# Kernel tuning notes

Measured on AMD Instinct MI355X. Metric: run time of the kernel, lower is better.

Reference implementation:

```python
import jax, jax.numpy as jnp
import numpy as np
import math

B, H, S, D = 2, 16, 2048, 72
D12 = D // 12  # freq dim per head per component
L_PREFIX, L_SEQ = 576, 512
THETA_T = 100.0


def _make_freqs():
    n = H * D12
    log_min, log_max = math.log(math.pi), math.log(10.0 * math.pi)
    f = jnp.exp(jnp.linspace(log_min, log_max, n + 1)[:-1])  # (H*D12,)
    freqs = jnp.stack([f, f]).reshape(2, D12, H)
    freqs = jnp.swapaxes(freqs, -1, -2)  # (2, H, D12)
    t = THETA_T ** (-jnp.arange(n, dtype=jnp.float32) / n)
    t_freqs = t.reshape(D12, H).T  # (H, D12)
    return freqs.astype(jnp.float32), t_freqs.astype(jnp.float32)


def setup_inputs() -> dict:
    key = jax.random.key(0)
    ks = jax.random.split(key, 8)
    freqs, t_freqs = _make_freqs()
    return {
        "q": jax.random.normal(ks[0], (B, H, S, D), dtype=jnp.float32),
        "k": jax.random.normal(ks[1], (B, H, S, D), dtype=jnp.float32),
        "v": jax.random.normal(ks[2], (B, H, S, D), dtype=jnp.float32),
        "pos": jax.random.uniform(ks[3], (B, S, 2), dtype=jnp.float32),
        "pos_orig": jax.random.uniform(ks[4], (B, S, 2), dtype=jnp.float32),
        "time": jax.random.uniform(ks[5], (B, S), dtype=jnp.float32),
        "freqs": freqs,
        "t_freqs": t_freqs,
        "scale": jax.random.uniform(ks[6], (H, 1, 1), dtype=jnpp_f32()) if False else jax.random.uniform(ks[6], (H, 1, 1), dtype=jnp.float32) + 0.5,
        "l_prefix": L_PREFIX,
        "l_seq": L_SEQ,
    }


def jnp_f32():
    return jnp.float32


def _fp_rope_theta(pos, pos_orig, time, freqs, t_freqs):
    # FPRoPE.forward: theta per token, per head. (B,S,H,5*D12)
    p = jnp.stack([pos_orig, pos], axis=2) * 2.0 - 1.0  # (B,S,2,2)
    th_w = p[..., 0][:, :, :, None, None] * freqs[0]  # (B,S,2,H,D12)
    th_h = p[..., 1][:, :, :, None, None] * freqs[1]  # (B,S,2,H,D12)
    th_t = time[:, :, None, None, None] * t_freqs      # (B,S,1,H,D12)
    theta = jnp.concatenate([th_h, th_w, th_t], axis=2)  # (B,S,5,H,D12)
    theta = jnp.transpose(theta, (0, 3, 1, 2, 4)).reshape(B, H, S, 5 * D12)
    return theta


def _apply_rotary(x, theta):
    d = theta.shape[-1]
    x1, x2, x3 = x[..., :d], x[..., d:2 * d], x[..., 2 * d:]
    c, s = jnp.cos(theta), jnp.sin(theta)
    return jnp.concatenate([x1 * c - x2 * s, x2 * c + x1 * s, x3], axis=-1)


def _block_mask(l_prefix, l_seq):
    # inference_query_causal_mask_mod: prefix attends to nothing; pokes causal;
    # queries attend to prefix+pokes (and self via qn==kn).
    idx = jnp.arange(S)
    qn = (idx - l_prefix)[:, None]
    kn = (idx - l_prefix)[None, :]
    return (qn >= 0) & ((qn == kn) | ((qn >= kn) & (qn < l_seq)) | ((kn < l_seq) & (qn >= l_seq)))


def reference(q, k, v, pos, pos_orig, time, freqs, t_freqs, scale, l_prefix, l_seq):
    theta = _fp_rope_theta(pos, pos_orig, time, freqs, t_freqs)
    q = _apply_rotary(q, theta)
    k = _apply_rotary(k, theta)
    # cosine-similarity QK rescaling (scale_for_cosine_sim)
    eps = 1e-6
    ss = jnp.sqrt(scale)  # (H,1,1) broadcasts over (B,H,S,1)
    q = q * (ss * jax.lax.rsqrt(jnp.sum(q * q, axis=-1, keepdims=True) + eps))
    k = k * (ss * jax.lax.rsqrt(jnp.sum(k * k, axis=-1, keepdims=True) + eps))
    mask = _block_mask(l_prefix, l_seq)  # (S,S)
    scores = jnp.einsum('bhqd,bhkd->bhqk', q, k)
    scores = jnp.where(mask, scores, jnp.float32(-1e30))
    probs = jax.nn.softmax(scores, axis=-1)
    # fully-masked rows (prefix queries) output zeros, matching flex_attention
    row_valid = jnp.any(mask, axis=-1)  # (S,)
    probs = jnp.where(row_valid[None, None, :, None], probs, 0.0)
    return jnp.einsum('bhqk,bhkd->bhqd', probs, v)
```

## Files before the change

kernel.cpp:

```cpp
#include <hip/hip_runtime.h>
#include <math.h>

#define B_ 2
#define H_ 16
#define S_ 2048
#define D_ 72
#define LP 576
#define WEND 1088
#define DP 96
#define DV 80
#define NQ (S_ - LP)

#define CBW 5376
#define LDSW (CBW + 256 + 64)

#define NPREP2 (B_ * H_ * S_ / 8)
#define NVT    (32 * B_ * H_)

typedef __bf16 bf16x8 __attribute__((ext_vector_type(8)));
typedef float f32x4 __attribute__((ext_vector_type(4)));

static __device__ __forceinline__ unsigned pack2bf(float a, float b) {
    __bf16 x = (__bf16)a, y = (__bf16)b;
    unsigned short ux = __builtin_bit_cast(unsigned short, x);
    unsigned short uy = __builtin_bit_cast(unsigned short, y);
    return (unsigned)ux | ((unsigned)uy << 16);
}

static __device__ __forceinline__ f32x4 mfma16(bf16x8 a, bf16x8 b, f32x4 c) {
    return __builtin_amdgcn_mfma_f32_16x16x32_bf16(a, b, c, 0, 0, 0);
}

__global__ __launch_bounds__(256) void pre_kernel(
    const float* __restrict__ q, const float* __restrict__ k,
    const float* __restrict__ v,
    const float* __restrict__ pos, const float* __restrict__ pos_orig,
    const float* __restrict__ time_, const float* __restrict__ freqs,
    const float* __restrict__ t_freqs, const float* __restrict__ scale,
    unsigned* __restrict__ qn, unsigned* __restrict__ kn,
    unsigned short* __restrict__ vt, float* __restrict__ out)
{
    __shared__ __align__(16) float tile[64 * 77];
    if (blockIdx.x < NPREP2) {
        unsigned short* shp = (unsigned short*)tile;
        const int wave = threadIdx.x >> 6;
        const int lane = threadIdx.x & 63;
        const int j = lane & 31;
        const int rw = wave * 2 + (lane >> 5);
        const int row = blockIdx.x * 8 + rw;
        const int s = row & (S_ - 1);
        const int h = (row >> 11) & (H_ - 1);
        const int b = row >> 15;
        const long base = (long)row * D_;
        const int p2 = (b * S_ + s) * 2;

        float oq1 = 0.f, oq2 = 0.f, ok1 = 0.f, ok2 = 0.f;
        float pq[6], pk[6];
        float ssq = 0.f, ssk = 0.f;
        if (j < 30) {
            const float x1q = q[base + j], x2q = q[base + j + 30];
            const float x1k = k[base + j], x2k = k[base + j + 30];
            const int g = j / 6, i = j - 6 * g;
            const float fh = freqs[96 + h * 6 + i];
            const float fw = freqs[h * 6 + i];
            const float ft = t_freqs[h * 6 + i];
            const float f  = (g < 2) ? fh : ((g < 4) ? fw : ft);
            const float by_o = pos_orig[p2 + 1] * 2.f - 1.f;
            const float by_p = pos[p2 + 1]      * 2.f - 1.f;
            const float bx_o = pos_orig[p2 + 0] * 2.f - 1.f;
            const float bx_p = pos[p2 + 0]      * 2.f - 1.f;
            const float bt   = time_[b * S_ + s];
            const float bv = (g == 0) ? by_o : (g == 1) ? by_p :
                             (g == 2) ? bx_o : (g == 3) ? bx_p : bt;
            float sn, cs;
            __sincosf(bv * f, &sn, &cs);
            oq1 = x1q * cs - x2q * sn;  oq2 = x2q * cs + x1q * sn;
            ok1 = x1k * cs - x2k * sn;  ok2 = x2k * cs + x1k * sn;
            ssq = oq1 * oq1 + oq2 * oq2;
            ssk = ok1 * ok1 + ok2 * ok2;
        } else {
            const int e0 = 60 + 6 * (j - 30);
            #pragma unroll
            for (int m = 0; m < 3; ++m) {
                const float2 a = *(const float2*)(q + base + e0 + 2 * m);
                const float2 c = *(const float2*)(k + base + e0 + 2 * m);
                pq[2 * m] = a.x; pq[2 * m + 1] = a.y;
                pk[2 * m] = c.x; pk[2 * m + 1] = c.y;
                ssq += a.x * a.x + a.y * a.y;
                ssk += c.x * c.x + c.y * c.y;
            }
        }
        #pragma unroll
        for (int m = 1; m < 32; m <<= 1) { ssq += __shfl_xor(ssq, m); ssk += __shfl_xor(ssk, m); }
        const float ss = sqrtf(scale[h]);
        const float fq = ss * rsqrtf(ssq + 1e-6f);
        const float fk = ss * rsqrtf(ssk + 1e-6f);

        unsigned short* sq_ = shp + rw * 96;
        unsigned short* sk_ = shp + 768 + rw * 96;
        if (j < 30) {
            sq_[j]      = __builtin_bit_cast(unsigned short, (__bf16)(oq1 * fq));
            sq_[j + 30] = __builtin_bit_cast(unsigned short, (__bf16)(oq2 * fq));
            sk_[j]      = __builtin_bit_cast(unsigned short, (__bf16)(ok1 * fk));
            sk_[j + 30] = __builtin_bit_cast(unsigned short, (__bf16)(ok2 * fk));
        } else {
            const int e0 = 60 + 6 * (j - 30);
            #pragma unroll
            for (int m = 0; m < 6; ++m) {
                sq_[e0 + m] = __builtin_bit_cast(unsigned short, (__bf16)(pq[m] * fq));
                sk_[e0 + m] = __builtin_bit_cast(unsigned short, (__bf16)(pk[m] * fk));
            }
        }
        __syncthreads();
        const int t = threadIdx.x;
        if (t < 192) {
            const int arr = t / 96, rem = t - arr * 96;
            const int rr = rem / 12, seg = rem - rr * 12;
            uint4 val = make_uint4(0u, 0u, 0u, 0u);
            if (seg < 9) val = ((const uint4*)(shp + arr * 768 + rr * 96))[seg];
            unsigned* dst = (arr ? kn : qn) + ((long)(blockIdx.x * 8 + rr)) * 48;
            ((uint4*)dst)[seg] = val;
        }
    } else {
        const int bx2 = blockIdx.x - NPREP2;
        const int st = bx2 & 31, bh = bx2 >> 5;
        const int s0 = st * 64;
        const int t = threadIdx.x;
        if (st < 9) {
            float4* o4 = (float4*)(out + (long)(bh * S_ + s0) * D_);
            for (int i = t; i < 1152; i += 256) o4[i] = make_float4(0.f, 0.f, 0.f, 0.f);
        }
        for (int i = t; i < 1152; i += 256) {
            const int r = i / 18, c = i - r * 18;
            const float4 g = ((const float4*)v)[((long)(bh * S_ + s0 + r) * 18) + c];
            float* d = &tile[r * 77 + c * 4];
            d[0] = g.x; d[1] = g.y; d[2] = g.z; d[3] = g.w;
        }
        __syncthreads();
        for (int i = t; i < 1280; i += 256) {
            const int dd = i >> 4, s4 = i & 15;
            float f0 = 0.f, f1 = 0.f, f2 = 0.f, f3 = 0.f;
            if (dd < D_) {
                f0 = tile[(s4 * 4 + 0) * 77 + dd];
                f1 = tile[(s4 * 4 + 1) * 77 + dd];
                f2 = tile[(s4 * 4 + 2) * 77 + dd];
                f3 = tile[(s4 * 4 + 3) * 77 + dd];
            }
            uint2 o; o.x = pack2bf(f0, f1); o.y = pack2bf(f2, f3);
            ((uint2*)vt)[((((long)bh * DV + dd) << 11) + s0 + s4 * 4) >> 2] = o;
        }
    }
}

__global__ __launch_bounds__(256) void attn_kernel(
    const unsigned short* __restrict__ qn, const unsigned short* __restrict__ kn,
    const unsigned short* __restrict__ vt, float* __restrict__ out)
{
    __shared__ __align__(16) unsigned lds[LDSW];
    const int bh = blockIdx.y;
    const int q0 = LP + blockIdx.x * 64;
    const int tid = threadIdx.x;
    const int w = tid >> 6, lane = tid & 63;
    const int quad = lane >> 4, l16 = lane & 15;
    const bool causal = (q0 < WEND);
    const int ntiles = causal ? ((q0 + 191) >> 7) : 9;

    const unsigned short* qn_b = qn + (((long)bh) << 11) * DP;
    const unsigned short* kn_b = kn + (((long)bh) << 11) * DP;
    const unsigned short* vt_b = vt + (long)bh * DV * S_;

    bf16x8 qf[4][3];
    #pragma unroll
    for (int m = 0; m < 4; ++m)
        #pragma unroll
        for (int c = 0; c < 3; ++c)
            qf[m][c] = *(const bf16x8*)(qn_b + (long)(q0 + 16 * m + l16) * DP + c * 32 + quad * 8);

    f32x4 o[4][5];
    float den[4][4];
    #pragma unroll
    for (int m = 0; m < 4; ++m) {
        #pragma unroll
        for (int dt = 0; dt < 5; ++dt) { o[m][dt][0]=0.f; o[m][dt][1]=0.f; o[m][dt][2]=0.f; o[m][dt][3]=0.f; }
        #pragma unroll
        for (int r = 0; r < 4; ++r) den[m][r] = 0.f;
    }

    unsigned short* Pw = (unsigned short*)lds + w * 640;

    for (int kt = 0; kt < ntiles; ++kt) {
        const int kb = kt * 128 + 32 * w;
        bf16x8 kf[2][3], vf[5];
        #pragma unroll
        for (int g = 0; g < 2; ++g)
            #pragma unroll
            for (int c = 0; c < 3; ++c)
                kf[g][c] = *(const bf16x8*)(kn_b + (long)(kb + 16 * g + l16) * DP + c * 32 + quad * 8);
        #pragma unroll
        for (int dt = 0; dt < 5; ++dt)
            vf[dt] = *(const bf16x8*)(vt_b + (((long)(dt * 16 + l16)) << 11) + kb + quad * 8);

        #pragma unroll
        for (int m = 0; m < 4; ++m) {
            f32x4 acc0, acc1;
            acc0[0]=0.f; acc0[1]=0.f; acc0[2]=0.f; acc0[3]=0.f;
            acc1[0]=0.f; acc1[1]=0.f; acc1[2]=0.f; acc1[3]=0.f;
            #pragma unroll
            for (int c = 0; c < 3; ++c) {
                acc0 = mfma16(qf[m][c], kf[0][c], acc0);
                acc1 = mfma16(qf[m][c], kf[1][c], acc1);
            }
            #pragma unroll
            for (int g = 0; g < 2; ++g) {
                const int ka = kb + 16 * g + l16;
                #pragma unroll
                for (int r = 0; r < 4; ++r) {
                    const int qa = q0 + 16 * m + quad * 4 + r;
                    float p = g ? acc1[r] : acc0[r];
                    const bool valid = causal ? (ka <= qa) : (ka < WEND);
                    p = valid ? __expf(p) : 0.f;
                    const __bf16 pb = (__bf16)p;
                    den[m][r] += (float)pb;
                    Pw[(quad * 4 + r) * 40 + 16 * g + l16] = __builtin_bit_cast(unsigned short, pb);
                }
            }
            const bf16x8 pa = *(const bf16x8*)(Pw + l16 * 40 + quad * 8);
            #pragma unroll
            for (int dt = 0; dt < 5; ++dt)
                o[m][dt] = mfma16(pa, vf[dt], o[m][dt]);
        }
    }

    #pragma unroll
    for (int m = 0; m < 4; ++m)
        #pragma unroll
        for (int r = 0; r < 4; ++r)
            #pragma unroll
            for (int x = 1; x < 16; x <<= 1) den[m][r] += __shfl_xor(den[m][r], x);

    __syncthreads();
    float* cb  = (float*)lds;
    float* db  = (float*)lds + CBW;
    float* PsD = (float*)lds + CBW + 256;
    if (l16 == 0)
        #pragma unroll
        for (int m = 0; m < 4; ++m)
            #pragma unroll
            for (int r = 0; r < 4; ++r)
                db[w * 64 + 16 * m + quad * 4 + r] = den[m][r];

    float ofin[5][4];
    #pragma unroll
    for (int dt = 0; dt < 5; ++dt) {
        __syncthreads();
        #pragma unroll
        for (int m = 0; m < 4; ++m)
            #pragma unroll
            for (int r = 0; r < 4; ++r)
                cb[w * 1344 + (16 * m + quad * 4 + r) * 21 + l16] = o[m][dt][r];
        __syncthreads();
        #pragma unroll
        for (int r = 0; r < 4; ++r) {
            const int row = 16 * w + quad * 4 + r;
            ofin[dt][r] = cb[row * 21 + l16] + cb[1344 + row * 21 + l16]
                        + cb[2688 + row * 21 + l16] + cb[4032 + row * 21 + l16];
        }
    }
    float dfin[4];
    #pragma unroll
    for (int r = 0; r < 4; ++r) {
        const int row = 16 * w + quad * 4 + r;
        dfin[r] = db[row] + db[64 + row] + db[128 + row] + db[192 + row];
    }

    if (!causal) {
        bf16x8 qw[3];
        #pragma unroll
        for (int m = 0; m < 4; ++m)
            if (w == m) { qw[0] = qf[m][0]; qw[1] = qf[m][1]; qw[2] = qf[m][2]; }
        float sp = 0.f;
        #pragma unroll
        for (int c = 0; c < 3; ++c) {
            const bf16x8 kd = *(const bf16x8*)(kn_b + (long)(q0 + 16 * w + l16) * DP + c * 32 + quad * 8);
            #pragma unroll
            for (int j = 0; j < 8; ++j) sp += (float)qw[c][j] * (float)kd[j];
        }
        sp += __shfl_xor(sp, 16);
        sp += __shfl_xor(sp, 32);
        if (quad == 0) PsD[w * 16 + l16] = __expf(sp);
        #pragma unroll
        for (int r = 0; r < 4; ++r) {
            const float pd = PsD[w * 16 + quad * 4 + r];
            dfin[r] += pd;
            const int qa = q0 + 16 * w + quad * 4 + r;
            #pragma unroll
            for (int dt = 0; dt < 5; ++dt) {
                const unsigned short uv = vt_b[(((long)(dt * 16 + l16)) << 11) + qa];
                ofin[dt][r] += pd * (float)__builtin_bit_cast(__bf16, uv);
            }
        }
    }

    #pragma unroll
    for (int r = 0; r < 4; ++r) {
        const float inv = 1.f / dfin[r];
        const int qa = q0 + 16 * w + quad * 4 + r;
        float* orow = out + ((long)(bh * S_ + qa)) * D_;
        #pragma unroll
        for (int dt = 0; dt < 5; ++dt) {
            const int dim = dt * 16 + l16;
            if (dim < D_) orow[dim] = ofin[dt][r] * inv;
        }
    }
}

extern "C" void kernel_launch(void* const* d_in, const int* in_sizes, int n_in,
                              void* d_out, int out_size, void* d_ws, size_t ws_size,
                              hipStream_t stream) {
    const float* q        = (const float*)d_in[0];
    const float* k        = (const float*)d_in[1];
    const float* v        = (const float*)d_in[2];
    const float* pos      = (const float*)d_in[3];
    const float* pos_orig = (const float*)d_in[4];
    const float* time_    = (const float*)d_in[5];
    const float* freqs    = (const float*)d_in[6];
    const float* t_freqs  = (const float*)d_in[7];
    const float* scale    = (const float*)d_in[8];
    float* out = (float*)d_out;

    unsigned* qn = (unsigned*)d_ws;
    unsigned* kn = qn + (size_t)B_ * H_ * S_ * 48;
    unsigned short* vt = (unsigned short*)(kn + (size_t)B_ * H_ * S_ * 48);

    pre_kernel<<<dim3(NPREP2 + NVT), dim3(256), 0, stream>>>(
        q, k, v, pos, pos_orig, time_, freqs, t_freqs, scale, qn, kn, vt, out);
    attn_kernel<<<dim3(NQ / 64, B_ * H_), dim3(256), 0, stream>>>(
        (const unsigned short*)qn, (const unsigned short*)kn, vt, out);
}
```

Before: 175.5 us.

## Double-buffer K/V tile loads in registers and mask only the last tile

Restructures the attention key loop to prefetch the next tile's K and V fragments into a second register buffer while the current tile is computed. Applies the causal/window mask only on the final tile instead of every tile. It also raises MFMA wave priority with s_setprio and requests 3 waves per SIMD through launch bounds. The extra register buffer plus the tighter occupancy bound raises register pressure and the risk of spills, and the last iteration issues one unused prefetch.

```diff
diff --git a/kernel.cpp b/kernel.cpp
--- a/kernel.cpp
+++ b/kernel.cpp
@@ -152,7 +152,7 @@
     }
 }
 
-__global__ __launch_bounds__(256) void attn_kernel(
+__global__ __launch_bounds__(256, 3) void attn_kernel(
     const unsigned short* __restrict__ qn, const unsigned short* __restrict__ kn,
     const unsigned short* __restrict__ vt, float* __restrict__ out)
 {
@@ -188,48 +188,73 @@
 
     unsigned short* Pw = (unsigned short*)lds + w * 640;
 
-    for (int kt = 0; kt < ntiles; ++kt) {
-        const int kb = kt * 128 + 32 * w;
-        bf16x8 kf[2][3], vf[5];
-        #pragma unroll
-        for (int g = 0; g < 2; ++g)
-            #pragma unroll
-            for (int c = 0; c < 3; ++c)
-                kf[g][c] = *(const bf16x8*)(kn_b + (long)(kb + 16 * g + l16) * DP + c * 32 + quad * 8);
-        #pragma unroll
-        for (int dt = 0; dt < 5; ++dt)
-            vf[dt] = *(const bf16x8*)(vt_b + (((long)(dt * 16 + l16)) << 11) + kb + quad * 8);
-
-        #pragma unroll
-        for (int m = 0; m < 4; ++m) {
-            f32x4 acc0, acc1;
-            acc0[0]=0.f; acc0[1]=0.f; acc0[2]=0.f; acc0[3]=0.f;
-            acc1[0]=0.f; acc1[1]=0.f; acc1[2]=0.f; acc1[3]=0.f;
-            #pragma unroll
-            for (int c = 0; c < 3; ++c) {
-                acc0 = mfma16(qf[m][c], kf[0][c], acc0);
-                acc1 = mfma16(qf[m][c], kf[1][c], acc1);
-            }
-            #pragma unroll
-            for (int g = 0; g < 2; ++g) {
-                const int ka = kb + 16 * g + l16;
-                #pragma unroll
-                for (int r = 0; r < 4; ++r) {
-                    const int qa = q0 + 16 * m + quad * 4 + r;
-                    float p = g ? acc1[r] : acc0[r];
-                    const bool valid = causal ? (ka <= qa) : (ka < WEND);
-                    p = valid ? __expf(p) : 0.f;
-                    const __bf16 pb = (__bf16)p;
-                    den[m][r] += (float)pb;
-                    Pw[(quad * 4 + r) * 40 + 16 * g + l16] = __builtin_bit_cast(unsigned short, pb);
-                }
-            }
-            const bf16x8 pa = *(const bf16x8*)(Pw + l16 * 40 + quad * 8);
-            #pragma unroll
-            for (int dt = 0; dt < 5; ++dt)
-                o[m][dt] = mfma16(pa, vf[dt], o[m][dt]);
-        }
-    }
+#define LOAD_TILE(KF, VF, KT) do {                                                           \
+    const int kb_ = (KT) * 128 + 32 * w;                                                     \
+    _Pragma("unroll")                                                                        \
+    for (int g = 0; g < 2; ++g) {                                                            \
+        _Pragma("unroll")                                                                    \
+        for (int c = 0; c < 3; ++c)                                                          \
+            KF[g][c] = *(const bf16x8*)(kn_b + (long)(kb_ + 16 * g + l16) * DP + c * 32 + quad * 8); \
+    }                                                                                        \
+    _Pragma("unroll")                                                                        \
+    for (int dt = 0; dt < 5; ++dt)                                                           \
+        VF[dt] = *(const bf16x8*)(vt_b + (((long)(dt * 16 + l16)) << 11) + kb_ + quad * 8);  \
+} while (0)
+
+#define COMP_TILE(KF, VF, KT) do {                                                           \
+    const int kb_ = (KT) * 128 + 32 * w;                                                     \
+    const bool masked_ = ((KT) == ntiles - 1);                                               \
+    _Pragma("unroll")                                                                        \
+    for (int m = 0; m < 4; ++m) {                                                            \
+        f32x4 acc0, acc1;                                                                    \
+        acc0[0]=0.f; acc0[1]=0.f; acc0[2]=0.f; acc0[3]=0.f;                                  \
+        acc1[0]=0.f; acc1[1]=0.f; acc1[2]=0.f; acc1[3]=0.f;                                  \
+        __builtin_amdgcn_s_setprio(1);                                                       \
+        _Pragma("unroll")                                                                    \
+        for (int c = 0; c < 3; ++c) {                                                        \
+            acc0 = mfma16(qf[m][c], KF[0][c], acc0);                                         \
+            acc1 = mfma16(qf[m][c], KF[1][c], acc1);                                         \
+        }                                                                                    \
+        __builtin_amdgcn_s_setprio(0);                                                       \
+        _Pragma("unroll")                                                                    \
+        for (int g = 0; g < 2; ++g) {                                                        \
+            const int ka = kb_ + 16 * g + l16;                                               \
+            _Pragma("unroll")                                                                \
+            for (int r = 0; r < 4; ++r) {                                                    \
+                const int qa = q0 + 16 * m + quad * 4 + r;                                   \
+                float p = g ? acc1[r] : acc0[r];                                             \
+                float e = __expf(p);                                                         \
+                if (masked_) {                                                               \
+                    const bool valid = causal ? (ka <= qa) : (ka < WEND);                    \
+                    if (!valid) e = 0.f;                                                     \
+                }                                                                            \
+                const __bf16 pb = (__bf16)e;                                                 \
+                den[m][r] += (float)pb;                                                      \
+                Pw[(quad * 4 + r) * 40 + 16 * g + l16] = __builtin_bit_cast(unsigned short, pb); \
+            }                                                                                \
+        }                                                                                    \
+        const bf16x8 pa = *(const bf16x8*)(Pw + l16 * 40 + quad * 8);                        \
+        __builtin_amdgcn_s_setprio(1);                                                       \
+        _Pragma("unroll")                                                                    \
+        for (int dt = 0; dt < 5; ++dt)                                                       \
+            o[m][dt] = mfma16(pa, VF[dt], o[m][dt]);                                         \
+        __builtin_amdgcn_s_setprio(0);                                                       \
+    }                                                                                        \
+} while (0)
+
+    bf16x8 kfA[2][3], vfA[5], kfB[2][3], vfB[5];
+    int kt = 0;
+    LOAD_TILE(kfA, vfA, 0);
+    for (;;) {
+        LOAD_TILE(kfB, vfB, kt + 1);
+        COMP_TILE(kfA, vfA, kt);
+        if (++kt == ntiles) break;
+        LOAD_TILE(kfA, vfA, kt + 1);
+        COMP_TILE(kfB, vfB, kt);
+        if (++kt == ntiles) break;
+    }
+#undef LOAD_TILE
+#undef COMP_TILE
 
     #pragma unroll
     for (int m = 0; m < 4; ++m)
```

New measurement: 348.8 us. 98.8% more time.
